# Kernel optimization log

Measured on AMD Instinct MI355X. Metric: run time of the kernel, lower is better.

The kernel has to match this reference:

```python
import jax, jax.numpy as jnp
import numpy as np

NEG_SLOPE = 0.2


def gat_conv(x, src, dst, W, att_src, att_dst, bias, heads, out_ch, concat, N):
    # Linear transform: [N, heads, out_ch]
    h = (x @ W).reshape(N, heads, out_ch)
    # Per-node attention logits [N, heads]
    a_s = jnp.einsum('nhc,hc->nh', h, att_src)
    a_d = jnp.einsum('nhc,hc->nh', h, att_dst)
    # Per-edge logits: edge j->i uses src j, dst i
    e = jax.nn.leaky_relu(a_s[src] + a_d[dst], NEG_SLOPE)  # [E, heads]
    # Segment softmax over destination neighborhoods
    m = jax.ops.segment_max(e, dst, num_segments=N)  # [N, heads]
    ex = jnp.exp(e - m[dst])
    denom = jax.ops.segment_sum(ex, dst, num_segments=N)
    alpha = ex / denom[dst]  # [E, heads]
    # Weighted message scatter-add
    out = jax.ops.segment_sum(h[src] * alpha[:, :, None], dst, num_segments=N)  # [N, heads, out_ch]
    out = out.reshape(N, heads * out_ch) if concat else out.mean(axis=1)
    return out + bias


def setup_inputs() -> dict:
    key = jax.random.key(0)
    ks = jax.random.split(key, 12)
    N, E, F_IN, HID, HEADS, NCLS = 100000, 1600000, 256, 16, 8, 32
    x = jax.random.normal(ks[0], (N, F_IN), dtype=jnp.float32)
    edge_index = jax.random.randint(ks[1], (2, E), 0, N, dtype=jnp.int32)
    edge_weight = jax.random.uniform(ks[2], (E,), dtype=jnp.float32)
    s1 = 1.0 / np.sqrt(F_IN)
    W1 = jax.random.normal(ks[3], (F_IN, HEADS * HID), dtype=jnp.float32) * s1
    att_src1 = jax.random.normal(ks[4], (HEADS, HID), dtype=jnp.float32) * 0.1
    att_dst1 = jax.random.normal(ks[5], (HEADS, HID), dtype=jnp.float32) * 0.1
    b1 = jnp.zeros((HEADS * HID,), dtype=jnp.float32)
    s2 = 1.0 / np.sqrt(HEADS * HID)
    W2 = jax.random.normal(ks[6], (HEADS * HID, NCLS), dtype=jnp.float32) * s2
    att_src2 = jax.random.normal(ks[7], (1, NCLS), dtype=jnp.float32) * 0.1
    att_dst2 = jax.random.normal(ks[8], (1, NCLS), dtype=jnp.float32) * 0.1
    b2 = jnp.zeros((NCLS,), dtype=jnp.float32)
    return {"x": x, "edge_index": edge_index, "edge_weight": edge_weight,
            "W1": W1, "att_src1": att_src1, "att_dst1": att_dst1, "b1": b1,
            "W2": W2, "att_src2": att_src2, "att_dst2": att_dst2, "b2": b2}


def reference(x, edge_index, edge_weight, W1, att_src1, att_dst1, b1, W2, att_src2, att_dst2, b2):
    N = x.shape[0]
    # PyG GATConv add_self_loops=True: append self-loops once (used by both layers)
    loop = jnp.arange(N, dtype=edge_index.dtype)
    src = jnp.concatenate([edge_index[0], loop])
    dst = jnp.concatenate([edge_index[1], loop])
    # eval mode: dropout is identity; edge_weight unused by GATConv
    h = gat_conv(x, src, dst, W1, att_src1, att_dst1, b1, heads=8, out_ch=16, concat=True, N=N)
    h = jax.nn.elu(h)
    out = gat_conv(h, src, dst, W2, att_src2, att_dst2, b2, heads=1, out_ch=32, concat=False, N=N)
    return jax.nn.log_softmax(out, axis=-1)
```

## Files before the change

kernel.cpp:

```cpp
#include <hip/hip_runtime.h>
#include <hip/hip_fp16.h>
#include <math.h>

#define NEG_SLOPE 0.2f
#define NBLK 256

typedef _Float16 half8 __attribute__((ext_vector_type(8)));
typedef _Float16 half4 __attribute__((ext_vector_type(4)));
typedef float f32x4 __attribute__((ext_vector_type(4)));
typedef float f32x2 __attribute__((ext_vector_type(2)));

__device__ __forceinline__ float lrelu(float x){ return x > 0.f ? x : NEG_SLOPE*x; }

__global__ void k_prepw(const float* __restrict__ W, _Float16* __restrict__ Wt){
  int t = blockIdx.x*blockDim.x + threadIdx.x;
  int p = t >> 8, k = t & 255;
  int c = ((p & 15) << 3) | (p >> 4);
  Wt[t] = (_Float16)W[k*128 + c];
}

__global__ __launch_bounds__(512) void k_gemm1(const float* __restrict__ x,
                                               const _Float16* __restrict__ Wt,
                                               const float* __restrict__ as_w,
                                               const float* __restrict__ ad_w,
                                               unsigned* __restrict__ h1p,
                                               float* __restrict__ a_s,
                                               float* __restrict__ a_d, int N){
  __shared__ _Float16 aL[2][128*40];
  __shared__ _Float16 bL[2][128*40];
  int tid = threadIdx.x;
  int w = tid >> 6, lane = tid & 63;
  int fq = lane >> 4, fr = lane & 15;
  int row0 = blockIdx.x * 128;
  f32x4 acc[8];
  #pragma unroll
  for (int n=0;n<8;n++) acc[n] = (f32x4){0.f,0.f,0.f,0.f};

  int rA = tid>>2, kcA = (tid&3)*8;
  float4 va0, va1; half8 vb;

  {
    int gr = row0 + rA;
    va0 = make_float4(0.f,0.f,0.f,0.f);
    va1 = make_float4(0.f,0.f,0.f,0.f);
    if (gr < N){
      va0 = *(const float4*)&x[(size_t)gr*256 + kcA];
      va1 = *(const float4*)&x[(size_t)gr*256 + kcA + 4];
    }
    vb = *(const half8*)&Wt[(size_t)rA*256 + kcA];
  }
  {
    half8 hv;
    hv[0]=(_Float16)va0.x; hv[1]=(_Float16)va0.y; hv[2]=(_Float16)va0.z; hv[3]=(_Float16)va0.w;
    hv[4]=(_Float16)va1.x; hv[5]=(_Float16)va1.y; hv[6]=(_Float16)va1.z; hv[7]=(_Float16)va1.w;
    *(half8*)&aL[0][rA*40 + kcA] = hv;
    *(half8*)&bL[0][rA*40 + kcA] = vb;
  }
  __syncthreads();

  int cur = 0;
  for (int ki=0; ki<8; ki++){
    int kk = ki*32;
    if (ki < 7){
      int gr = row0 + rA;
      va0 = make_float4(0.f,0.f,0.f,0.f);
      va1 = make_float4(0.f,0.f,0.f,0.f);
      if (gr < N){
        va0 = *(const float4*)&x[(size_t)gr*256 + kk + 32 + kcA];
        va1 = *(const float4*)&x[(size_t)gr*256 + kk + 32 + kcA + 4];
      }
      vb = *(const half8*)&Wt[(size_t)rA*256 + kk + 32 + kcA];
    }
    int kb = fq*8;
    half8 afrag = *(half8*)&aL[cur][(w*16 + fr)*40 + kb];
    half8 bfrag[8];
    #pragma unroll
    for (int n=0;n<8;n++) bfrag[n] = *(half8*)&bL[cur][(n*16 + fr)*40 + kb];
    #pragma unroll
    for (int n=0;n<8;n++)
      acc[n] = __builtin_amdgcn_mfma_f32_16x16x32_f16(afrag, bfrag[n], acc[n], 0, 0, 0);
    if (ki < 7){
      half8 hv;
      hv[0]=(_Float16)va0.x; hv[1]=(_Float16)va0.y; hv[2]=(_Float16)va0.z; hv[3]=(_Float16)va0.w;
      hv[4]=(_Float16)va1.x; hv[5]=(_Float16)va1.y; hv[6]=(_Float16)va1.z; hv[7]=(_Float16)va1.w;
      *(half8*)&aL[cur^1][rA*40 + kcA] = hv;
      *(half8*)&bL[cur^1][rA*40 + kcA] = vb;
      __syncthreads();
      cur ^= 1;
    }
  }
  int head = fr >> 1;
  const float* wsp = &as_w[head*16 + (fr&1)*8];
  const float* wdp = &ad_w[head*16 + (fr&1)*8];
  #pragma unroll
  for (int j=0;j<4;j++){
    int gr = row0 + w*16 + fq*4 + j;
    if (gr < N){
      float f[8];
      #pragma unroll
      for (int n=0;n<8;n++) f[n] = acc[n][j];
      int w0 = 0, w1 = 0;
      w0 = __builtin_amdgcn_cvt_pk_fp8_f32(f[0], f[1], w0, false);
      w0 = __builtin_amdgcn_cvt_pk_fp8_f32(f[2], f[3], w0, true);
      w1 = __builtin_amdgcn_cvt_pk_fp8_f32(f[4], f[5], w1, false);
      w1 = __builtin_amdgcn_cvt_pk_fp8_f32(f[6], f[7], w1, true);
      *(uint2*)&h1p[(size_t)gr*32 + fr*2] = make_uint2((unsigned)w0,(unsigned)w1);
      float s=0.f, dd=0.f;
      #pragma unroll
      for (int n=0;n<8;n++){ s = fmaf(f[n], wsp[n], s); dd = fmaf(f[n], wdp[n], dd); }
      s  += __shfl_xor(s, 1);
      dd += __shfl_xor(dd, 1);
      if (!(fr & 1)){ a_s[(size_t)gr*8+head] = s; a_d[(size_t)gr*8+head] = dd; }
    }
  }
}

__global__ __launch_bounds__(256) void k_bh(const int* __restrict__ dst, int* __restrict__ bh,
                                            int E, int EE, int NB){
  __shared__ int h[1024];
  int tid = threadIdx.x, blk = blockIdx.x;
  for (int i=tid;i<1024;i+=256) h[i]=0;
  __syncthreads();
  int chunk = (EE + NBLK - 1)/NBLK;
  int e0 = blk*chunk, e1 = min(e0+chunk, EE);
  for (int e=e0+tid; e<e1; e+=256){
    int d = (e<E)? dst[e] : (e-E);
    atomicAdd(&h[d>>7], 1);
  }
  __syncthreads();
  for (int i=tid;i<NB;i+=256) bh[i*NBLK + blk] = h[i];
}

__global__ __launch_bounds__(256) void k_scanA(int* __restrict__ bh, int* __restrict__ btot){
  __shared__ int t[256];
  int b = blockIdx.x, tid = threadIdx.x;
  int v = bh[b*NBLK + tid];
  t[tid] = v;
  __syncthreads();
  for (int off=1; off<256; off<<=1){
    int p = (tid>=off)? t[tid-off] : 0;
    __syncthreads();
    t[tid] += p;
    __syncthreads();
  }
  bh[b*NBLK + tid] = t[tid] - v;
  if (tid==255) btot[b] = t[255];
}

__global__ __launch_bounds__(256) void k_bscan(const int* __restrict__ btot, int* __restrict__ bbase,
                                               int* __restrict__ start_, int NB, int N, int EE){
  __shared__ int t[256];
  int tid = threadIdx.x;
  int i0 = tid*4;
  int a0 = (i0+0<NB)? btot[i0+0] : 0;
  int a1 = (i0+1<NB)? btot[i0+1] : 0;
  int a2 = (i0+2<NB)? btot[i0+2] : 0;
  int a3 = (i0+3<NB)? btot[i0+3] : 0;
  int s = a0+a1+a2+a3;
  t[tid] = s;
  __syncthreads();
  for (int off=1; off<256; off<<=1){
    int p = (tid>=off)? t[tid-off] : 0;
    __syncthreads();
    t[tid] += p;
    __syncthreads();
  }
  int excl = t[tid] - s;
  int e0=excl, e1=e0+a0, e2=e1+a1, e3=e2+a2;
  if (i0+0<NB) bbase[i0+0]=e0;
  if (i0+1<NB) bbase[i0+1]=e1;
  if (i0+2<NB) bbase[i0+2]=e2;
  if (i0+3<NB) bbase[i0+3]=e3;
  if (tid==0){ bbase[NB] = EE; start_[N] = EE; }
}

__global__ __launch_bounds__(256) void k_bfill(const int* __restrict__ src, const int* __restrict__ dst,
                       const int* __restrict__ bh, const int* __restrict__ bbase,
                       unsigned* __restrict__ pairs, int E, int EE, int NB){
  __shared__ int cur[1024];
  int tid = threadIdx.x, blk = blockIdx.x;
  for (int i=tid;i<NB;i+=256) cur[i] = bbase[i] + bh[i*NBLK + blk];
  __syncthreads();
  int chunk = (EE + NBLK - 1)/NBLK;
  int e0 = blk*chunk, e1 = min(e0+chunk, EE);
  for (int e=e0+tid; e<e1; e+=256){
    int s,d;
    if (e<E){ s=src[e]; d=dst[e]; } else { s=e-E; d=s; }
    int p = atomicAdd(&cur[d>>7], 1);
    pairs[p] = ((unsigned)s << 7) | (unsigned)(d & 127);
  }
}

__global__ __launch_bounds__(256) void k_pb(const int* __restrict__ bbase, const unsigned* __restrict__ pairs,
                    int* __restrict__ start_, int* __restrict__ csr_src, int N){
  __shared__ int hist[128];
  __shared__ int excl[128];
  int b = blockIdx.x;
  int tid = threadIdx.x;
  int base = bbase[b], cnt = bbase[b+1] - base;
  if (tid<128) hist[tid]=0;
  __syncthreads();
  for (int i=tid;i<cnt;i+=256){
    unsigned p = pairs[base+i];
    atomicAdd(&hist[p & 127], 1);
  }
  __syncthreads();
  if (tid < 128) excl[tid] = hist[tid];
  __syncthreads();
  for (int off=1; off<128; off<<=1){
    int p=0;
    if (tid<128 && tid>=off) p = excl[tid-off];
    __syncthreads();
    if (tid<128) excl[tid] += p;
    __syncthreads();
  }
  if (tid < 128){
    int e = excl[tid] - hist[tid];
    int node = (b<<7) + tid;
    if (node < N) start_[node] = base + e;
    hist[tid] = e;
  }
  __syncthreads();
  for (int i=tid;i<cnt;i+=256){
    unsigned p = pairs[base+i];
    int pos = atomicAdd(&hist[p & 127], 1);
    csr_src[base + pos] = (int)(p >> 7);
  }
}

__global__ __launch_bounds__(256) void k_agg1(const int* __restrict__ start, const int* __restrict__ csr_src,
                      const float* __restrict__ a_s, const float* __restrict__ a_d,
                      const unsigned* __restrict__ h1p, _Float16* __restrict__ acc1h, int N){
  int wid = (blockIdx.x*blockDim.x + threadIdx.x) >> 6;
  int lane = threadIdx.x & 63;
  if (wid >= N) return;
  int d = wid;
  int grp = lane >> 4;
  int fr  = lane & 15;
  int head = fr >> 1;
  float ad = a_d[(size_t)d*8 + head];
  int beg = start[d], end = start[d+1];
  float a0=0.f,a1=0.f,a2=0.f,a3=0.f,a4=0.f,a5=0.f,a6=0.f,a7=0.f,den=0.f;
  int j = beg + grp;
  for (; j + 4 < end; j += 8){
    int s0 = csr_src[j];
    int s1 = csr_src[j+4];
    float e0 = __expf(lrelu(a_s[(size_t)s0*8 + head] + ad));
    float e1 = __expf(lrelu(a_s[(size_t)s1*8 + head] + ad));
    uint2 u0 = *(const uint2*)&h1p[(size_t)s0*32 + fr*2];
    uint2 u1 = *(const uint2*)&h1p[(size_t)s1*32 + fr*2];
    f32x2 p0 = __builtin_amdgcn_cvt_pk_f32_fp8((int)u0.x, false), p1 = __builtin_amdgcn_cvt_pk_f32_fp8((int)u0.x, true);
    f32x2 p2 = __builtin_amdgcn_cvt_pk_f32_fp8((int)u0.y, false), p3 = __builtin_amdgcn_cvt_pk_f32_fp8((int)u0.y, true);
    f32x2 q0 = __builtin_amdgcn_cvt_pk_f32_fp8((int)u1.x, false), q1 = __builtin_amdgcn_cvt_pk_f32_fp8((int)u1.x, true);
    f32x2 q2 = __builtin_amdgcn_cvt_pk_f32_fp8((int)u1.y, false), q3 = __builtin_amdgcn_cvt_pk_f32_fp8((int)u1.y, true);
    a0 = fmaf(e0, p0.x, a0); a1 = fmaf(e0, p0.y, a1); a2 = fmaf(e0, p1.x, a2); a3 = fmaf(e0, p1.y, a3);
    a4 = fmaf(e0, p2.x, a4); a5 = fmaf(e0, p2.y, a5); a6 = fmaf(e0, p3.x, a6); a7 = fmaf(e0, p3.y, a7);
    a0 = fmaf(e1, q0.x, a0); a1 = fmaf(e1, q0.y, a1); a2 = fmaf(e1, q1.x, a2); a3 = fmaf(e1, q1.y, a3);
    a4 = fmaf(e1, q2.x, a4); a5 = fmaf(e1, q2.y, a5); a6 = fmaf(e1, q3.x, a6); a7 = fmaf(e1, q3.y, a7);
    den += e0 + e1;
  }
  if (j < end){
    int s0 = csr_src[j];
    float e0 = __expf(lrelu(a_s[(size_t)s0*8 + head] + ad));
    uint2 u0 = *(const uint2*)&h1p[(size_t)s0*32 + fr*2];
    f32x2 p0 = __builtin_amdgcn_cvt_pk_f32_fp8((int)u0.x, false), p1 = __builtin_amdgcn_cvt_pk_f32_fp8((int)u0.x, true);
    f32x2 p2 = __builtin_amdgcn_cvt_pk_f32_fp8((int)u0.y, false), p3 = __builtin_amdgcn_cvt_pk_f32_fp8((int)u0.y, true);
    a0 = fmaf(e0, p0.x, a0); a1 = fmaf(e0, p0.y, a1); a2 = fmaf(e0, p1.x, a2); a3 = fmaf(e0, p1.y, a3);
    a4 = fmaf(e0, p2.x, a4); a5 = fmaf(e0, p2.y, a5); a6 = fmaf(e0, p3.x, a6); a7 = fmaf(e0, p3.y, a7);
    den += e0;
  }
  a0 += __shfl_xor(a0,16); a1 += __shfl_xor(a1,16); a2 += __shfl_xor(a2,16); a3 += __shfl_xor(a3,16);
  a4 += __shfl_xor(a4,16); a5 += __shfl_xor(a5,16); a6 += __shfl_xor(a6,16); a7 += __shfl_xor(a7,16);
  den += __shfl_xor(den,16);
  a0 += __shfl_xor(a0,32); a1 += __shfl_xor(a1,32); a2 += __shfl_xor(a2,32); a3 += __shfl_xor(a3,32);
  a4 += __shfl_xor(a4,32); a5 += __shfl_xor(a5,32); a6 += __shfl_xor(a6,32); a7 += __shfl_xor(a7,32);
  den += __shfl_xor(den,32);
  float inv = (den > 0.f) ? 1.f/den : 0.f;
  if (grp == 0){
    half8 o;
    o[0]=(_Float16)(a0*inv); o[1]=(_Float16)(a1*inv); o[2]=(_Float16)(a2*inv); o[3]=(_Float16)(a3*inv);
    o[4]=(_Float16)(a4*inv); o[5]=(_Float16)(a5*inv); o[6]=(_Float16)(a6*inv); o[7]=(_Float16)(a7*inv);
    *(half8*)&acc1h[(size_t)d*128 + fr*8] = o;
  }
}

__global__ __launch_bounds__(256) void k_layer2(const _Float16* __restrict__ acc1h, const float* __restrict__ b1,
                        const float* __restrict__ W2, const float* __restrict__ as2w,
                        const float* __restrict__ ad2w,
                        __half* __restrict__ h2ph, float* __restrict__ a_s2,
                        float* __restrict__ a_d2, int N){
  __shared__ float w2s[128][32];
  __shared__ float hs[8][128];
  int tid = threadIdx.x;
  #pragma unroll
  for (int it=0; it<16; it++){
    int idx = it*256 + tid;
    ((float*)w2s)[idx] = W2[idx];
  }
  int sub = tid>>5, ln = tid&31;
  int n = blockIdx.x*8 + sub;
  if (n < N){
    half4 hv = *(const half4*)&acc1h[(size_t)n*128 + ln*4];
    float4 bb = *(const float4*)&b1[ln*4];
    float v0 = (float)hv[0] + bb.x;
    float v1 = (float)hv[1] + bb.y;
    float v2 = (float)hv[2] + bb.z;
    float v3 = (float)hv[3] + bb.w;
    hs[sub][ln*4+0] = v0 > 0.f ? v0 : (__expf(v0) - 1.f);
    hs[sub][ln*4+1] = v1 > 0.f ? v1 : (__expf(v1) - 1.f);
    hs[sub][ln*4+2] = v2 > 0.f ? v2 : (__expf(v2) - 1.f);
    hs[sub][ln*4+3] = v3 > 0.f ? v3 : (__expf(v3) - 1.f);
  }
  __syncthreads();
  if (n >= N) return;
  float o = 0.f;
  #pragma unroll
  for (int k=0;k<128;k++) o = fmaf(hs[sub][k], w2s[k][ln], o);
  h2ph[(size_t)n*32+ln] = __float2half_rn(o);
  float ps = o*as2w[ln], pd = o*ad2w[ln];
  #pragma unroll
  for (int m=16;m;m>>=1){ ps += __shfl_xor(ps,m); pd += __shfl_xor(pd,m); }
  if (ln==0){ a_s2[n]=ps; a_d2[n]=pd; }
}

__global__ __launch_bounds__(256) void k_agg2(const int* __restrict__ start, const int* __restrict__ csr_src,
                      const float* __restrict__ a_s2, const float* __restrict__ a_d2,
                      const __half* __restrict__ h2ph, const float* __restrict__ b2,
                      float* __restrict__ out, int N){
  int g = (blockIdx.x*blockDim.x + threadIdx.x) >> 5;
  int ln = threadIdx.x & 31;
  if (g >= N) return;
  int d = g;
  int grp = ln >> 4;
  int l16 = ln & 15;
  float ad = a_d2[d];
  int beg = start[d], end = start[d+1];
  float accx=0.f, accy=0.f, den=0.f;
  int j = beg + grp;
  for (; j + 6 < end; j += 8){
    int s0 = csr_src[j];
    int s1 = csr_src[j+2];
    int s2 = csr_src[j+4];
    int s3 = csr_src[j+6];
    float e0 = __expf(lrelu(a_s2[s0] + ad));
    float e1 = __expf(lrelu(a_s2[s1] + ad));
    float e2 = __expf(lrelu(a_s2[s2] + ad));
    float e3 = __expf(lrelu(a_s2[s3] + ad));
    float2 v0 = __half22float2(*(const __half2*)&h2ph[(size_t)s0*32 + l16*2]);
    float2 v1 = __half22float2(*(const __half2*)&h2ph[(size_t)s1*32 + l16*2]);
    float2 v2 = __half22float2(*(const __half2*)&h2ph[(size_t)s2*32 + l16*2]);
    float2 v3 = __half22float2(*(const __half2*)&h2ph[(size_t)s3*32 + l16*2]);
    accx = fmaf(e0, v0.x, accx); accy = fmaf(e0, v0.y, accy);
    accx = fmaf(e1, v1.x, accx); accy = fmaf(e1, v1.y, accy);
    accx = fmaf(e2, v2.x, accx); accy = fmaf(e2, v2.y, accy);
    accx = fmaf(e3, v3.x, accx); accy = fmaf(e3, v3.y, accy);
    den += (e0 + e1) + (e2 + e3);
  }
  for (; j < end; j += 2){
    int s0 = csr_src[j];
    float e0 = __expf(lrelu(a_s2[s0] + ad));
    float2 v0 = __half22float2(*(const __half2*)&h2ph[(size_t)s0*32 + l16*2]);
    accx = fmaf(e0, v0.x, accx); accy = fmaf(e0, v0.y, accy);
    den += e0;
  }
  accx += __shfl_xor(accx, 16);
  accy += __shfl_xor(accy, 16);
  den  += __shfl_xor(den, 16);
  float2 bb = *(const float2*)&b2[l16*2];
  float vx = accx/den + bb.x;
  float vy = accy/den + bb.y;
  float mx = fmaxf(vx, vy);
  #pragma unroll
  for (int m=8;m;m>>=1) mx = fmaxf(mx, __shfl_xor(mx, m));
  float sm = __expf(vx-mx) + __expf(vy-mx);
  #pragma unroll
  for (int m=8;m;m>>=1) sm += __shfl_xor(sm, m);
  float lg = mx + __logf(sm);
  if (grp == 0){
    float2 o = make_float2(vx - lg, vy - lg);
    *(float2*)&out[(size_t)d*32 + l16*2] = o;
  }
}

extern "C" void kernel_launch(void* const* d_in, const int* in_sizes, int n_in,
                              void* d_out, int out_size, void* d_ws, size_t ws_size,
                              hipStream_t stream){
  const float* x   = (const float*)d_in[0];
  const int*   ei  = (const int*)d_in[1];
  const float* W1  = (const float*)d_in[3];
  const float* as1 = (const float*)d_in[4];
  const float* ad1 = (const float*)d_in[5];
  const float* b1  = (const float*)d_in[6];
  const float* W2  = (const float*)d_in[7];
  const float* as2 = (const float*)d_in[8];
  const float* ad2 = (const float*)d_in[9];
  const float* b2  = (const float*)d_in[10];

  int N  = in_sizes[0] / 256;
  int E  = in_sizes[2];
  int EE = E + N;
  const int* src = ei;
  const int* dst = ei + E;

  int NB = (N + 127) >> 7;

  int* iw = (int*)d_ws;
  int* bh      = iw;                 iw += 1024*NBLK;
  int* btot    = iw;                 iw += 1024;
  int* bbase   = iw;                 iw += 1028;
  int* start_  = iw;                 iw += ((N+1+3)/4)*4;
  int* csr_src = iw;                 iw += ((EE+3)/4)*4;

  float* w = (float*)iw;
  float* a_s1   = w; w += (size_t)N*8;
  float* a_d1   = w; w += (size_t)N*8;
  float* a_s2   = w; w += (size_t)N;
  float* a_d2   = w; w += (size_t)N;
  _Float16* acc1h = (_Float16*)w; w += (size_t)N*64;
  _Float16* h2ph = (_Float16*)w; w += (size_t)N*16;
  _Float16* Wt   = (_Float16*)w; w += 32768/2;
  unsigned* h1p  = (unsigned*)w; w += (size_t)N*16;
  float* out    = (float*)d_out;

  unsigned* pairs = (unsigned*)acc1h;

  hipLaunchKernelGGL(k_prepw, dim3(128), dim3(256), 0, stream, W1, Wt);
  hipLaunchKernelGGL(k_gemm1, dim3((N+127)/128), dim3(512), 0, stream, x, Wt, as1, ad1, h1p, a_s1, a_d1, N);
  hipLaunchKernelGGL(k_bh,    dim3(NBLK), dim3(256), 0, stream, dst, bh, E, EE, NB);
  hipLaunchKernelGGL(k_scanA, dim3(NB),   dim3(256), 0, stream, bh, btot);
  hipLaunchKernelGGL(k_bscan, dim3(1),    dim3(256), 0, stream, btot, bbase, start_, NB, N, EE);
  hipLaunchKernelGGL(k_bfill, dim3(NBLK), dim3(256), 0, stream, src, dst, bh, bbase, pairs, E, EE, NB);
  hipLaunchKernelGGL(k_pb,    dim3(NB),   dim3(256), 0, stream, bbase, pairs, start_, csr_src, N);
  hipLaunchKernelGGL(k_agg1, dim3((N+3)/4), dim3(256), 0, stream, start_, csr_src, a_s1, a_d1, h1p, acc1h, N);
  hipLaunchKernelGGL(k_layer2, dim3((N+7)/8), dim3(256), 0, stream, acc1h, b1, W2, as2, ad2, (__half*)h2ph, a_s2, a_d2, N);
  hipLaunchKernelGGL(k_agg2, dim3((N+7)/8), dim3(256), 0, stream, start_, csr_src, a_s2, a_d2, (const __half*)h2ph, b2, out, N);
}
```

Measured before the change: 242.3 us.

## Load GEMM1 operands directly from global into MFMA fragments, dropping LDS staging

The first-layer GEMM no longer stages x and the transposed weights through double-buffered shared memory. Each wave reads its own A fragment rows from x and its B fragments from the small fp16 weight matrix straight from global memory (expected to hit in cache), with no block barriers. This removes the LDS writes, reads and syncthreads, but each wave now re-reads all of W from L2/L1 and loses the explicit prefetch overlap between tiles.

```diff
diff --git a/kernel.cpp b/kernel.cpp
--- a/kernel.cpp
+++ b/kernel.cpp
@@ -26,68 +26,36 @@
                                                unsigned* __restrict__ h1p,
                                                float* __restrict__ a_s,
                                                float* __restrict__ a_d, int N){
-  __shared__ _Float16 aL[2][128*40];
-  __shared__ _Float16 bL[2][128*40];
   int tid = threadIdx.x;
   int w = tid >> 6, lane = tid & 63;
   int fq = lane >> 4, fr = lane & 15;
   int row0 = blockIdx.x * 128;
+  int gra = row0 + w*16 + fr;
+  bool valid = gra < N;
+  const float* xrow = &x[(size_t)(valid ? gra : 0)*256 + fq*8];
+  const _Float16* wb = &Wt[(size_t)fr*256 + fq*8];
+
   f32x4 acc[8];
   #pragma unroll
   for (int n=0;n<8;n++) acc[n] = (f32x4){0.f,0.f,0.f,0.f};
 
-  int rA = tid>>2, kcA = (tid&3)*8;
-  float4 va0, va1; half8 vb;
-
-  {
-    int gr = row0 + rA;
-    va0 = make_float4(0.f,0.f,0.f,0.f);
-    va1 = make_float4(0.f,0.f,0.f,0.f);
-    if (gr < N){
-      va0 = *(const float4*)&x[(size_t)gr*256 + kcA];
-      va1 = *(const float4*)&x[(size_t)gr*256 + kcA + 4];
+  #pragma unroll 2
+  for (int ki=0; ki<8; ki++){
+    float4 a0 = make_float4(0.f,0.f,0.f,0.f);
+    float4 a1 = make_float4(0.f,0.f,0.f,0.f);
+    if (valid){
+      a0 = *(const float4*)&xrow[ki*32];
+      a1 = *(const float4*)&xrow[ki*32 + 4];
     }
-    vb = *(const half8*)&Wt[(size_t)rA*256 + kcA];
-  }
-  {
-    half8 hv;
-    hv[0]=(_Float16)va0.x; hv[1]=(_Float16)va0.y; hv[2]=(_Float16)va0.z; hv[3]=(_Float16)va0.w;
-    hv[4]=(_Float16)va1.x; hv[5]=(_Float16)va1.y; hv[6]=(_Float16)va1.z; hv[7]=(_Float16)va1.w;
-    *(half8*)&aL[0][rA*40 + kcA] = hv;
-    *(half8*)&bL[0][rA*40 + kcA] = vb;
-  }
-  __syncthreads();
-
-  int cur = 0;
-  for (int ki=0; ki<8; ki++){
-    int kk = ki*32;
-    if (ki < 7){
-      int gr = row0 + rA;
-      va0 = make_float4(0.f,0.f,0.f,0.f);
-      va1 = make_float4(0.f,0.f,0.f,0.f);
-      if (gr < N){
-        va0 = *(const float4*)&x[(size_t)gr*256 + kk + 32 + kcA];
-        va1 = *(const float4*)&x[(size_t)gr*256 + kk + 32 + kcA + 4];
-      }
-      vb = *(const half8*)&Wt[(size_t)rA*256 + kk + 32 + kcA];
-    }
-    int kb = fq*8;
-    half8 afrag = *(half8*)&aL[cur][(w*16 + fr)*40 + kb];
-    half8 bfrag[8];
+    half8 af;
+    af[0]=(_Float16)a0.x; af[1]=(_Float16)a0.y; af[2]=(_Float16)a0.z; af[3]=(_Float16)a0.w;
+    af[4]=(_Float16)a1.x; af[5]=(_Float16)a1.y; af[6]=(_Float16)a1.z; af[7]=(_Float16)a1.w;
+    half8 bf[8];
     #pragma unroll
-    for (int n=0;n<8;n++) bfrag[n] = *(half8*)&bL[cur][(n*16 + fr)*40 + kb];
+    for (int n=0;n<8;n++) bf[n] = *(const half8*)&wb[(size_t)n*4096 + ki*32];
     #pragma unroll
     for (int n=0;n<8;n++)
-      acc[n] = __builtin_amdgcn_mfma_f32_16x16x32_f16(afrag, bfrag[n], acc[n], 0, 0, 0);
-    if (ki < 7){
-      half8 hv;
-      hv[0]=(_Float16)va0.x; hv[1]=(_Float16)va0.y; hv[2]=(_Float16)va0.z; hv[3]=(_Float16)va0.w;
-      hv[4]=(_Float16)va1.x; hv[5]=(_Float16)va1.y; hv[6]=(_Float16)va1.z; hv[7]=(_Float16)va1.w;
-      *(half8*)&aL[cur^1][rA*40 + kcA] = hv;
-      *(half8*)&bL[cur^1][rA*40 + kcA] = vb;
-      __syncthreads();
-      cur ^= 1;
-    }
+      acc[n] = __builtin_amdgcn_mfma_f32_16x16x32_f16(af, bf[n], acc[n], 0, 0, 0);
   }
   int head = fr >> 1;
   const float* wsp = &as_w[head*16 + (fr&1)*8];
```

After: 291.4 us. 1.2x slower.

## Precompute per-edge exp attention weights in separate kernels before aggregation

Applied to the files above, without the earlier changes.

Splits edge-weight computation out of both aggregation kernels. New kernels k_w1 and k_w2 compute exp(leaky_relu(a_s[src]+a_d[dst])) per CSR edge and store it (fp16 for layer 1, fp32 for layer 2), and the aggregation kernels then read these contiguous values instead of gathering a_s and recomputing exp. The aim is to take the random a_s gathers and exp math off the aggregation critical path. The cost is two extra launches, an extra pass of random a_s gathers, and extra write and read traffic for the edge-weight arrays (about 27 MB for layer 1), plus fp16 rounding of the layer-1 weights.

```diff
diff --git a/kernel.cpp b/kernel.cpp
--- a/kernel.cpp
+++ b/kernel.cpp
@@ -228,8 +228,28 @@
   }
 }
 
+__global__ __launch_bounds__(256) void k_w1(const int* __restrict__ start, const int* __restrict__ csr_src,
+                    const float* __restrict__ a_s, const float* __restrict__ a_d,
+                    _Float16* __restrict__ w1, int N){
+  int wid = (blockIdx.x*blockDim.x + threadIdx.x) >> 6;
+  int lane = threadIdx.x & 63;
+  if (wid >= N) return;
+  int d = wid;
+  int le = lane >> 3, h = lane & 7;
+  float ad = a_d[(size_t)d*8 + h];
+  int beg = start[d], end = start[d+1];
+  for (int j0 = beg; j0 < end; j0 += 8){
+    int j = j0 + le;
+    if (j < end){
+      int s = csr_src[j];
+      float v = __expf(lrelu(a_s[(size_t)s*8 + h] + ad));
+      w1[(size_t)j*8 + h] = (_Float16)v;
+    }
+  }
+}
+
 __global__ __launch_bounds__(256) void k_agg1(const int* __restrict__ start, const int* __restrict__ csr_src,
-                      const float* __restrict__ a_s, const float* __restrict__ a_d,
+                      const _Float16* __restrict__ w1,
                       const unsigned* __restrict__ h1p, _Float16* __restrict__ acc1h, int N){
   int wid = (blockIdx.x*blockDim.x + threadIdx.x) >> 6;
   int lane = threadIdx.x & 63;
@@ -238,15 +258,14 @@
   int grp = lane >> 4;
   int fr  = lane & 15;
   int head = fr >> 1;
-  float ad = a_d[(size_t)d*8 + head];
   int beg = start[d], end = start[d+1];
   float a0=0.f,a1=0.f,a2=0.f,a3=0.f,a4=0.f,a5=0.f,a6=0.f,a7=0.f,den=0.f;
   int j = beg + grp;
   for (; j + 4 < end; j += 8){
     int s0 = csr_src[j];
     int s1 = csr_src[j+4];
-    float e0 = __expf(lrelu(a_s[(size_t)s0*8 + head] + ad));
-    float e1 = __expf(lrelu(a_s[(size_t)s1*8 + head] + ad));
+    float e0 = (float)w1[(size_t)j*8 + head];
+    float e1 = (float)w1[(size_t)(j+4)*8 + head];
     uint2 u0 = *(const uint2*)&h1p[(size_t)s0*32 + fr*2];
     uint2 u1 = *(const uint2*)&h1p[(size_t)s1*32 + fr*2];
     f32x2 p0 = __builtin_amdgcn_cvt_pk_f32_fp8((int)u0.x, false), p1 = __builtin_amdgcn_cvt_pk_f32_fp8((int)u0.x, true);
@@ -261,7 +280,7 @@
   }
   if (j < end){
     int s0 = csr_src[j];
-    float e0 = __expf(lrelu(a_s[(size_t)s0*8 + head] + ad));
+    float e0 = (float)w1[(size_t)j*8 + head];
     uint2 u0 = *(const uint2*)&h1p[(size_t)s0*32 + fr*2];
     f32x2 p0 = __builtin_amdgcn_cvt_pk_f32_fp8((int)u0.x, false), p1 = __builtin_amdgcn_cvt_pk_f32_fp8((int)u0.x, true);
     f32x2 p2 = __builtin_amdgcn_cvt_pk_f32_fp8((int)u0.y, false), p3 = __builtin_amdgcn_cvt_pk_f32_fp8((int)u0.y, true);
@@ -323,8 +342,23 @@
   if (ln==0){ a_s2[n]=ps; a_d2[n]=pd; }
 }
 
+__global__ __launch_bounds__(256) void k_w2(const int* __restrict__ start, const int* __restrict__ csr_src,
+                    const float* __restrict__ a_s2, const float* __restrict__ a_d2,
+                    float* __restrict__ w2a, int N){
+  int wid = (blockIdx.x*blockDim.x + threadIdx.x) >> 6;
+  int lane = threadIdx.x & 63;
+  if (wid >= N) return;
+  int d = wid;
+  float ad = a_d2[d];
+  int beg = start[d], end = start[d+1];
+  for (int j = beg + lane; j < end; j += 64){
+    int s = csr_src[j];
+    w2a[j] = __expf(lrelu(a_s2[s] + ad));
+  }
+}
+
 __global__ __launch_bounds__(256) void k_agg2(const int* __restrict__ start, const int* __restrict__ csr_src,
-                      const float* __restrict__ a_s2, const float* __restrict__ a_d2,
+                      const float* __restrict__ w2a,
                       const __half* __restrict__ h2ph, const float* __restrict__ b2,
                       float* __restrict__ out, int N){
   int g = (blockIdx.x*blockDim.x + threadIdx.x) >> 5;
@@ -333,7 +367,6 @@
   int d = g;
   int grp = ln >> 4;
   int l16 = ln & 15;
-  float ad = a_d2[d];
   int beg = start[d], end = start[d+1];
   float accx=0.f, accy=0.f, den=0.f;
   int j = beg + grp;
@@ -342,10 +375,10 @@
     int s1 = csr_src[j+2];
     int s2 = csr_src[j+4];
     int s3 = csr_src[j+6];
-    float e0 = __expf(lrelu(a_s2[s0] + ad));
-    float e1 = __expf(lrelu(a_s2[s1] + ad));
-    float e2 = __expf(lrelu(a_s2[s2] + ad));
-    float e3 = __expf(lrelu(a_s2[s3] + ad));
+    float e0 = w2a[j];
+    float e1 = w2a[j+2];
+    float e2 = w2a[j+4];
+    float e3 = w2a[j+6];
     float2 v0 = __half22float2(*(const __half2*)&h2ph[(size_t)s0*32 + l16*2]);
     float2 v1 = __half22float2(*(const __half2*)&h2ph[(size_t)s1*32 + l16*2]);
     float2 v2 = __half22float2(*(const __half2*)&h2ph[(size_t)s2*32 + l16*2]);
@@ -358,7 +391,7 @@
   }
   for (; j < end; j += 2){
     int s0 = csr_src[j];
-    float e0 = __expf(lrelu(a_s2[s0] + ad));
+    float e0 = w2a[j];
     float2 v0 = __half22float2(*(const __half2*)&h2ph[(size_t)s0*32 + l16*2]);
     accx = fmaf(e0, v0.x, accx); accy = fmaf(e0, v0.y, accy);
     den += e0;
@@ -416,9 +449,11 @@
   float* a_d1   = w; w += (size_t)N*8;
   float* a_s2   = w; w += (size_t)N;
   float* a_d2   = w; w += (size_t)N;
+  float* w2a    = w; w += ((size_t)EE+3)/4*4;
   _Float16* acc1h = (_Float16*)w; w += (size_t)N*64;
   _Float16* h2ph = (_Float16*)w; w += (size_t)N*16;
   _Float16* Wt   = (_Float16*)w; w += 32768/2;
+  _Float16* w1   = (_Float16*)w; w += (size_t)EE*4;
   unsigned* h1p  = (unsigned*)w; w += (size_t)N*16;
   float* out    = (float*)d_out;
 
@@ -431,7 +466,9 @@
   hipLaunchKernelGGL(k_bscan, dim3(1),    dim3(256), 0, stream, btot, bbase, start_, NB, N, EE);
   hipLaunchKernelGGL(k_bfill, dim3(NBLK), dim3(256), 0, stream, src, dst, bh, bbase, pairs, E, EE, NB);
   hipLaunchKernelGGL(k_pb,    dim3(NB),   dim3(256), 0, stream, bbase, pairs, start_, csr_src, N);
-  hipLaunchKernelGGL(k_agg1, dim3((N+3)/4), dim3(256), 0, stream, start_, csr_src, a_s1, a_d1, h1p, acc1h, N);
+  hipLaunchKernelGGL(k_w1,   dim3((N+3)/4), dim3(256), 0, stream, start_, csr_src, a_s1, a_d1, w1, N);
+  hipLaunchKernelGGL(k_agg1, dim3((N+3)/4), dim3(256), 0, stream, start_, csr_src, w1, h1p, acc1h, N);
   hipLaunchKernelGGL(k_layer2, dim3((N+7)/8), dim3(256), 0, stream, acc1h, b1, W2, as2, ad2, (__half*)h2ph, a_s2, a_d2, N);
-  hipLaunchKernelGGL(k_agg2, dim3((N+7)/8), dim3(256), 0, stream, start_, csr_src, a_s2, a_d2, (const __half*)h2ph, b2, out, N);
-}
+  hipLaunchKernelGGL(k_w2,   dim3((N+3)/4), dim3(256), 0, stream, start_, csr_src, a_s2, a_d2, w2a, N);
+  hipLaunchKernelGGL(k_agg2, dim3((N+7)/8), dim3(256), 0, stream, start_, csr_src, w2a, (const __half*)h2ph, b2, out, N);
+}
```

Result: slower. 277.5 us (+14.5%).
